# Kernel optimization log

Measured on AMD Instinct MI355X. Metric: run time of the kernel, lower is better.

Reference implementation:

```python
import jax, jax.numpy as jnp
import numpy as np

DIM = 3072
HEADS = 24
HD = 128
FF = 4 * DIM
EPS = 1e-6
SCALE_SHIFT = 1.0


def _ln(x):
    # LayerNorm, elementwise_affine=False
    mu = jnp.mean(x, axis=-1, keepdims=True)
    var = jnp.mean(jnp.square(x - mu), axis=-1, keepdims=True)
    return (x - mu) * jax.lax.rsqrt(var + EPS)


def _rms(x, w):
    # RMSNorm over head_dim with learned weight
    ms = jnp.mean(jnp.square(x), axis=-1, keepdims=True)
    return x * jax.lax.rsqrt(ms + EPS) * w


def _rope(x, cos, sin):
    # x: [B,S,H,D], cos/sin: [S,D]; interleaved rotate-half (diffusers style)
    xr = x.reshape(*x.shape[:-1], -1, 2)
    x1, x2 = xr[..., 0], xr[..., 1]
    rot = jnp.stack([-x2, x1], axis=-1).reshape(x.shape)
    return x * cos[None, :, None, :] + rot * sin[None, :, None, :]


def _mod_params(temb, w, b):
    m = jax.nn.silu(temb) @ w + b  # [B, 6*DIM]
    B = m.shape[0]
    m = m.reshape(B, -1, 6).transpose(0, 2, 1).reshape(B, -1)  # reorder to 6 blocks of DIM
    return jnp.split(m, 2, axis=-1)  # mod1, mod2 each [B, 3*DIM]


def _modulate(x, mp):
    shift, scale, gate = jnp.split(mp, 3, axis=-1)
    scale = scale + SCALE_SHIFT
    return x * scale[:, None, :] + shift[:, None, :], gate[:, None, :]


def setup_inputs() -> dict:
    key = jax.random.key(0)
    ks = jax.random.split(key, 32)
    B, ST, SI = 1, 512, 1024
    S = ST + SI
    r = lambda k, shp, s=1.0: jax.random.normal(k, shp, dtype=jnp.float32) * s
    W = 0.02  # weight init scale
    ang = jax.random.uniform(ks[5], (S, HD), minval=0.0, maxval=2 * np.pi)
    inp = {
        "hidden_states": r(ks[0], (B, SI, DIM)),
        "encoder_hidden_states": r(ks[1], (B, ST, DIM)),
        "encoder_hidden_states_mask": jnp.ones((B, ST), jnp.float32),
        "temb": r(ks[2], (B, DIM)),
        "rope_cos": jnp.cos(ang),
        "rope_sin": jnp.sin(ang),
        "w_img_mod": r(ks[6], (DIM, 6 * DIM), W), "b_img_mod": r(ks[7], (6 * DIM,), W),
        "w_txt_mod": r(ks[8], (DIM, 6 * DIM), W), "b_txt_mod": r(ks[9], (6 * DIM,), W),
        "norm_q_w": jnp.ones((HD,), jnp.float32), "norm_k_w": jnp.ones((HD,), jnp.float32),
        "norm_added_q_w": jnp.ones((HD,), jnp.float32), "norm_added_k_w": jnp.ones((HD,), jnp.float32),
        "w_qkv": r(ks[10], (DIM, 3 * DIM), W), "b_qkv": r(ks[11], (3 * DIM,), W),
        "w_add_qkv": r(ks[12], (DIM, 3 * DIM), W), "b_add_qkv": r(ks[13], (3 * DIM,), W),
        "w_out": r(ks[14], (DIM, DIM), W), "b_out": r(ks[15], (DIM,), W),
        "w_add_out": r(ks[16], (DIM, DIM), W), "b_add_out": r(ks[17], (DIM,), W),
        "w_img_mlp1": r(ks[18], (DIM, FF), W), "b_img_mlp1": r(ks[19], (FF,), W),
        "w_img_mlp2": r(ks[20], (FF, DIM), W), "b_img_mlp2": r(ks[21], (DIM,), W),
        "w_txt_mlp1": r(ks[22], (DIM, FF), W), "b_txt_mlp1": r(ks[23], (FF,), W),
        "w_txt_mlp2": r(ks[24], (FF, DIM), W), "b_txt_mlp2": r(ks[25], (DIM,), W),
    }
    return inp


def reference(hidden_states, encoder_hidden_states, encoder_hidden_states_mask, temb,
              rope_cos, rope_sin,
              w_img_mod, b_img_mod, w_txt_mod, b_txt_mod,
              norm_q_w, norm_k_w, norm_added_q_w, norm_added_k_w,
              w_qkv, b_qkv, w_add_qkv, b_add_qkv,
              w_out, b_out, w_add_out, b_add_out,
              w_img_mlp1, b_img_mlp1, w_img_mlp2, b_img_mlp2,
              w_txt_mlp1, b_txt_mlp1, w_txt_mlp2, b_txt_mlp2):
    B, SI, _ = hidden_states.shape
    ST = encoder_hidden_states.shape[1]

    img_mod1, img_mod2 = _mod_params(temb, w_img_mod, b_img_mod)
    txt_mod1, txt_mod2 = _mod_params(temb, w_txt_mod, b_txt_mod)

    img_m, img_g1 = _modulate(_ln(hidden_states), img_mod1)
    txt_m, txt_g1 = _modulate(_ln(encoder_hidden_states), txt_mod1)

    # joint attention
    iq, ik, iv = jnp.split(img_m @ w_qkv + b_qkv, 3, axis=-1)
    tq, tk, tv = jnp.split(txt_m @ w_add_qkv + b_add_qkv, 3, axis=-1)
    iq = _rms(iq.reshape(B, SI, HEADS, HD), norm_q_w)
    ik = _rms(ik.reshape(B, SI, HEADS, HD), norm_k_w)
    iv = iv.reshape(B, SI, HEADS, HD)
    tq = _rms(tq.reshape(B, ST, HEADS, HD), norm_added_q_w)
    tk = _rms(tk.reshape(B, ST, HEADS, HD), norm_added_k_w)
    tv = tv.reshape(B, ST, HEADS, HD)
    q = jnp.concatenate([tq, iq], axis=1)  # [B,S,H,D], txt first
    k = jnp.concatenate([tk, ik], axis=1)
    v = jnp.concatenate([tv, iv], axis=1)
    q = _rope(q, rope_cos, rope_sin)
    k = _rope(k, rope_cos, rope_sin)
    scores = jnp.einsum('bqhd,bkhd->bhqk', q, k) / np.float32(np.sqrt(HD))
    probs = jax.nn.softmax(scores, axis=-1)
    attn = jnp.einsum('bhqk,bkhd->bqhd', probs, v).reshape(B, ST + SI, HEADS * HD)

    txt_a = attn[:, :ST] @ w_add_out + b_add_out
    img_a = attn[:, ST:] @ w_out + b_out
    hidden = hidden_states + img_g1 * img_a
    enc = encoder_hidden_states + txt_g1 * txt_a

    # fused GELU(tanh) MLPs with modulation
    img_m2, img_g2 = _modulate(_ln(hidden), img_mod2)
    img_mlp = jax.nn.gelu(img_m2 @ w_img_mlp1 + b_img_mlp1, approximate=True) @ w_img_mlp2 + b_img_mlp2
    hidden = hidden + img_g2 * img_mlp

    txt_m2, txt_g2 = _modulate(_ln(enc), txt_mod2)
    txt_mlp = jax.nn.gelu(txt_m2 @ w_txt_mlp1 + b_txt_mlp1, approximate=True) @ w_txt_mlp2 + b_txt_mlp2
    enc = enc + txt_g2 * txt_mlp

    return enc, hidden
```

## Files before the change

kernel.cpp:

```cpp
#include <hip/hip_runtime.h>

#define DIMX 3072
#define STX 512
#define SIX 1024
#define SQX 1536
#define FFX 12288

typedef __attribute__((ext_vector_type(4))) float f32x4;
typedef __attribute__((ext_vector_type(8))) __bf16 bf16x8;
typedef __attribute__((ext_vector_type(4))) int i32x4;
typedef __attribute__((ext_vector_type(4))) unsigned short u16x4;

__device__ __forceinline__ unsigned short f2bf(float f){
  unsigned u = __builtin_bit_cast(unsigned, f);
  u += 0x7FFFu + ((u>>16)&1u);
  return (unsigned short)(u>>16);
}
__device__ __forceinline__ unsigned short usbf(float x){
  return __builtin_bit_cast(unsigned short, (__bf16)x);
}
__device__ __forceinline__ float bf2f(unsigned short h){
  unsigned u = ((unsigned)h)<<16;
  return __builtin_bit_cast(float, u);
}
__device__ __forceinline__ float gelu_tanh(float x){
  float x3 = x*x*x;
  float z = 0.7978845608028654f*(x + 0.044715f*x3);
  z = fminf(fmaxf(z, -15.f), 15.f);
  float e = exp2f(z*2.8853900817779268f);
  float th = (e-1.f)/(e+1.f);
  return 0.5f*x*(1.f+th);
}

__device__ __forceinline__ void gload16(const void* g, void* l){
  __builtin_amdgcn_global_load_lds(
      (const __attribute__((address_space(1))) void*)g,
      (__attribute__((address_space(3))) void*)l,
      16, 0, 0);
}


__global__ void k_silu(const float* __restrict__ temb, float* __restrict__ out){
  int i = blockIdx.x*256 + threadIdx.x;
  if(i < DIMX){
    float x = temb[i];
    out[i] = x / (1.f + exp2f(-x*1.4426950408889634f));
  }
}

__global__ void k_modinit(const float* __restrict__ b_img, const float* __restrict__ b_txt,
                          float* __restrict__ mod){
  int idx = blockIdx.x*256 + threadIdx.x;
  int mat = idx / 18432; int r = idx % 18432;
  int i = r/6, j = r%6;
  const float* b = mat ? b_txt : b_img;
  mod[mat*18432 + j*3072 + i] = b[r];
}

__global__ void k_modgemv(const float* __restrict__ w_img, const float* __restrict__ w_txt,
                          const float* __restrict__ silu_t, float* __restrict__ mod){
  int bz = blockIdx.x;
  int ks = bz & 7; bz >>= 3;
  int nc = bz % 18; int mat = bz / 18;
  const float* W = mat ? w_txt : w_img;
  __shared__ float st[384];
  int k0 = ks*384;
  for(int i = threadIdx.x; i < 384; i += 256) st[i] = silu_t[k0+i];
  __syncthreads();
  int n0 = nc*1024 + threadIdx.x*4;
  float ax=0.f, ay=0.f, az=0.f, aw=0.f;
  const float* Wp = W + (size_t)k0*18432 + n0;
  #pragma unroll 4
  for(int k=0;k<384;k++){
    float4 w = *(const float4*)(Wp + (size_t)k*18432);
    float s = st[k];
    ax += s*w.x; ay += s*w.y; az += s*w.z; aw += s*w.w;
  }
  float* md = mod + mat*18432;
  float vals[4] = {ax, ay, az, aw};
  #pragma unroll
  for(int j=0;j<4;j++){
    int n = n0+j; int i = n/6, jj = n%6;
    atomicAdd(&md[jj*3072 + i], vals[j]);
  }
}

__global__ void k_initC2(float* __restrict__ out0, const float* __restrict__ res0,
                         const float* __restrict__ gate0, const float* __restrict__ bias0,
                         float* __restrict__ out1, const float* __restrict__ res1,
                         const float* __restrict__ gate1, const float* __restrict__ bias1,
                         int R0){
  long i = ((long)blockIdx.x*256 + threadIdx.x)*4;
  int row = (int)(i / 3072);
  int col = (int)(i % 3072);
  const float* res; const float* gate; const float* bias; float* out;
  long off;
  if(row < R0){ res=res0; gate=gate0; bias=bias0; out=out0; off=i; }
  else        { res=res1; gate=gate1; bias=bias1; out=out1; off=i - (long)R0*3072; }
  float4 r = *(const float4*)(res + off);
  float4 g = *(const float4*)(gate + col);
  float4 b = *(const float4*)(bias + col);
  float4 o = {r.x + g.x*b.x, r.y + g.y*b.y, r.z + g.z*b.z, r.w + g.w*b.w};
  *(float4*)(out + off) = o;
}

__global__ void k_lnmod2(const float* __restrict__ x0, const float* __restrict__ modp0,
                         unsigned short* __restrict__ out0,
                         const float* __restrict__ x1, const float* __restrict__ modp1,
                         unsigned short* __restrict__ out1, int R0){
  int row = blockIdx.x, t = threadIdx.x;
  const float* x; const float* modp; unsigned short* out;
  if(row < R0){ x=x0; modp=modp0; out=out0; }
  else        { x=x1; modp=modp1; out=out1; row -= R0; }
  const float* xr = x + (size_t)row*DIMX;
  float4 v0 = *(const float4*)(xr + t*4);
  float4 v1 = *(const float4*)(xr + 1024 + t*4);
  float4 v2 = *(const float4*)(xr + 2048 + t*4);
  float s  = v0.x+v0.y+v0.z+v0.w + v1.x+v1.y+v1.z+v1.w + v2.x+v2.y+v2.z+v2.w;
  float s2 = v0.x*v0.x+v0.y*v0.y+v0.z*v0.z+v0.w*v0.w
           + v1.x*v1.x+v1.y*v1.y+v1.z*v1.z+v1.w*v1.w
           + v2.x*v2.x+v2.y*v2.y+v2.z*v2.z+v2.w*v2.w;
  #pragma unroll
  for(int o=32;o>0;o>>=1){ s += __shfl_xor(s,o); s2 += __shfl_xor(s2,o); }
  __shared__ float rs_[4], rs2_[4];
  int wid = t>>6;
  if((t&63)==0){ rs_[wid]=s; rs2_[wid]=s2; }
  __syncthreads();
  float S  = rs_[0]+rs_[1]+rs_[2]+rs_[3];
  float S2 = rs2_[0]+rs2_[1]+rs2_[2]+rs2_[3];
  float mu = S*(1.f/3072.f);
  float var = S2*(1.f/3072.f) - mu*mu;
  float rstd = rsqrtf(var + 1e-6f);
  #pragma unroll
  for(int j=0;j<3;j++){
    int c = j*1024 + t*4;
    float4 sh = *(const float4*)(modp + c);
    float4 sc = *(const float4*)(modp + 3072 + c);
    float4 xv = (j==0)?v0:((j==1)?v1:v2);
    unsigned short h0 = f2bf((xv.x-mu)*rstd*(sc.x+1.f)+sh.x);
    unsigned short h1 = f2bf((xv.y-mu)*rstd*(sc.y+1.f)+sh.y);
    unsigned short h2 = f2bf((xv.z-mu)*rstd*(sc.z+1.f)+sh.z);
    unsigned short h3 = f2bf((xv.w-mu)*rstd*(sc.w+1.f)+sh.w);
    unsigned long long pk = (unsigned long long)(h0 | ((unsigned)h1<<16))
                          | ((unsigned long long)(h2 | ((unsigned)h3<<16))<<32);
    *(unsigned long long*)(out + (size_t)row*DIMX + c) = pk;
  }
}

__global__ void k_rmsrope(const unsigned short* __restrict__ qkv_txt,
                          const unsigned short* __restrict__ qkv_img,
                          const float* __restrict__ nqw, const float* __restrict__ nkw,
                          const float* __restrict__ naqw, const float* __restrict__ nakw,
                          const float* __restrict__ cosb, const float* __restrict__ sinb,
                          unsigned short* __restrict__ Q, unsigned short* __restrict__ K,
                          unsigned short* __restrict__ V){
  int s = blockIdx.x, h = blockIdx.y, t = threadIdx.x;
  bool txt = s < STX;
  const unsigned short* src = txt ? (qkv_txt + (size_t)s*9216)
                                  : (qkv_img + (size_t)(s-STX)*9216);
  const float* qw = txt ? naqw : nqw;
  const float* kw = txt ? nakw : nkw;
  int d0 = 2*t;
  float q1 = bf2f(src[h*128 + d0]),        q2 = bf2f(src[h*128 + d0 + 1]);
  float k1 = bf2f(src[3072 + h*128 + d0]), k2 = bf2f(src[3072 + h*128 + d0 + 1]);
  float v1 = bf2f(src[6144 + h*128 + d0]), v2 = bf2f(src[6144 + h*128 + d0 + 1]);
  float sq = q1*q1 + q2*q2, sk = k1*k1 + k2*k2;
  #pragma unroll
  for(int o=32;o>0;o>>=1){ sq += __shfl_xor(sq,o); sk += __shfl_xor(sk,o); }
  float rq = rsqrtf(sq*(1.f/128.f) + 1e-6f);
  float rk = rsqrtf(sk*(1.f/128.f) + 1e-6f);
  q1 *= rq*qw[d0]; q2 *= rq*qw[d0+1];
  k1 *= rk*kw[d0]; k2 *= rk*kw[d0+1];
  float c1 = cosb[(size_t)s*128 + d0], c2 = cosb[(size_t)s*128 + d0 + 1];
  float s1 = sinb[(size_t)s*128 + d0], s2 = sinb[(size_t)s*128 + d0 + 1];
  float Q1 = q1*c1 - q2*s1, Q2 = q2*c2 + q1*s2;
  float K1 = k1*c1 - k2*s1, K2 = k2*c2 + k1*s2;
  size_t o = ((size_t)s*24 + h)*128 + d0;
  Q[o] = f2bf(Q1); Q[o+1] = f2bf(Q2);
  K[o] = f2bf(K1); K[o+1] = f2bf(K2);
  V[o] = f2bf(v1); V[o+1] = f2bf(v2);
}

__global__ void k_vtrans(const unsigned short* __restrict__ V, unsigned short* __restrict__ VT){
  __shared__ unsigned short tile[64][136];
  int st = blockIdx.x, h = blockIdx.y, t = threadIdx.x;
  int s0 = st*64;
  {
    int s = t>>2;
    #pragma unroll
    for(int i=0;i<4;i++){
      int oct = ((t&3)<<2) + i;
      i32x4 d = *(const i32x4*)(V + ((size_t)(s0+s)*24 + h)*128 + oct*8);
      *(i32x4*)&tile[s][oct*8] = d;
    }
  }
  __syncthreads();
  {
    int d0 = t>>3; int strip = t&7;
    #pragma unroll
    for(int i=0;i<4;i++){
      int d = d0 + i*32;
      unsigned short h8[8];
      #pragma unroll
      for(int j=0;j<8;j++) h8[j] = tile[strip*8 + j][d];
      unsigned a0 = h8[0] | ((unsigned)h8[1]<<16);
      unsigned a1 = h8[2] | ((unsigned)h8[3]<<16);
      unsigned a2 = h8[4] | ((unsigned)h8[5]<<16);
      unsigned a3 = h8[6] | ((unsigned)h8[7]<<16);
      i32x4 dv = {(int)a0,(int)a1,(int)a2,(int)a3};
      *(i32x4*)(VT + ((size_t)h*128 + d)*1536 + s0 + strip*8) = dv;
    }
  }
}

__global__ __launch_bounds__(256,2) void k_fattn(
    const unsigned short* __restrict__ Q,
    const unsigned short* __restrict__ Kb,
    const unsigned short* __restrict__ VT,
    unsigned short* __restrict__ O)
{
  __shared__ unsigned short Kls[4][64][32];
  __shared__ unsigned short Vls[2][128][32];
  __shared__ unsigned short Pls[128][72];
  const int t = threadIdx.x;
  const int qb = blockIdx.x, h = blockIdx.y;
  const int lane = t&63, w = t>>6;
  const int lr = lane&15, lk = lane>>4;
  const float SC  = 0.08838834764831845f;
  const float L2E = 1.4426950408889634f;
  const int schunk = ((lane&3) ^ ((lane>>2)&3))*8;
  const int rswz   = ((lr&3)<<3);

  bf16x8 qf[2][4];
  {
    const unsigned short* qp = Q + ((size_t)(qb*128 + w*32 + lr)*3072) + h*128 + lk*8;
    #pragma unroll
    for(int mf=0;mf<2;mf++)
      #pragma unroll
      for(int ks=0;ks<4;ks++)
        qf[mf][ks] = *(const bf16x8*)(qp + (size_t)mf*16*3072 + ks*32);
  }

  f32x4 o[2][8];
  #pragma unroll
  for(int i=0;i<2;i++)
    #pragma unroll
    for(int j=0;j<8;j++) o[i][j] = (f32x4){0.f,0.f,0.f,0.f};
  float mrow[2][4], lrow[2][4];
  #pragma unroll
  for(int i=0;i<2;i++)
    #pragma unroll
    for(int r=0;r<4;r++){ mrow[i][r] = -3.0e30f; lrow[i][r] = 0.f; }

  for(int kv0=0; kv0<SQX; kv0+=64){
    __syncthreads();
    {
      const unsigned short* kp = Kb + ((size_t)(kv0 + (lane>>2))*3072) + h*128 + w*32 + schunk;
      #pragma unroll
      for(int i=0;i<4;i++)
        gload16(kp + (size_t)i*16*3072, &Kls[w][i*16][0]);
    }
    {
      int c = w>>1;
      const unsigned short* vp = VT + ((size_t)(h*128 + (w&1)*64 + (lane>>2)))*1536 + kv0 + c*32 + schunk;
      #pragma unroll
      for(int j=0;j<4;j++)
        gload16(vp + (size_t)j*16*1536, &Vls[c][(w&1)*64 + j*16][0]);
    }
    __syncthreads();

    f32x4 s[2][4];
    #pragma unroll
    for(int mf=0;mf<2;mf++)
      #pragma unroll
      for(int nf=0;nf<4;nf++) s[mf][nf] = (f32x4){0.f,0.f,0.f,0.f};
    #pragma unroll
    for(int ks=0;ks<4;ks++){
      bf16x8 kf[4];
      #pragma unroll
      for(int nf=0;nf<4;nf++) kf[nf] = *(const bf16x8*)&Kls[ks][nf*16+lr][(lk*8) ^ rswz];
      #pragma unroll
      for(int mf=0;mf<2;mf++)
        #pragma unroll
        for(int nf=0;nf<4;nf++)
          s[mf][nf] = __builtin_amdgcn_mfma_f32_16x16x32_bf16(qf[mf][ks], kf[nf], s[mf][nf], 0,0,0);
    }

    #pragma unroll
    for(int mf=0;mf<2;mf++){
      #pragma unroll
      for(int r=0;r<4;r++){
        float v = fmaxf(fmaxf(s[mf][0][r], s[mf][1][r]), fmaxf(s[mf][2][r], s[mf][3][r]));
        #pragma unroll
        for(int d=1; d<16; d<<=1) v = fmaxf(v, __shfl_xor(v, d));
        float nm = fmaxf(mrow[mf][r], v*SC);
        float fac = exp2f((mrow[mf][r]-nm)*L2E);
        mrow[mf][r] = nm;
        float rs = 0.f;
        #pragma unroll
        for(int nf=0;nf<4;nf++){
          float p = exp2f((s[mf][nf][r]*SC - nm)*L2E);
          s[mf][nf][r] = p;
          rs += p;
        }
        #pragma unroll
        for(int d=1; d<16; d<<=1) rs += __shfl_xor(rs, d);
        lrow[mf][r] = lrow[mf][r]*fac + rs;
        #pragma unroll
        for(int nf=0;nf<8;nf++) o[mf][nf][r] *= fac;
      }
    }

    #pragma unroll
    for(int mf=0;mf<2;mf++)
      #pragma unroll
      for(int nf=0;nf<4;nf++)
        #pragma unroll
        for(int r=0;r<4;r++)
          Pls[w*32 + mf*16 + lk*4 + r][nf*16 + lr] = usbf(s[mf][nf][r]);

    #pragma unroll
    for(int ks2=0; ks2<2; ks2++){
      bf16x8 pa[2];
      #pragma unroll
      for(int mf=0;mf<2;mf++)
        pa[mf] = *(const bf16x8*)&Pls[w*32 + mf*16 + lr][ks2*32 + lk*8];
      #pragma unroll
      for(int nf=0;nf<8;nf++){
        bf16x8 vf = *(const bf16x8*)&Vls[ks2][nf*16+lr][(lk*8) ^ rswz];
        #pragma unroll
        for(int mf=0;mf<2;mf++)
          o[mf][nf] = __builtin_amdgcn_mfma_f32_16x16x32_bf16(pa[mf], vf, o[mf][nf], 0,0,0);
      }
    }
  }

  #pragma unroll
  for(int mf=0;mf<2;mf++){
    float inv[4];
    #pragma unroll
    for(int r=0;r<4;r++) inv[r] = 1.f/lrow[mf][r];
    #pragma unroll
    for(int nf=0;nf<8;nf++){
      #pragma unroll
      for(int r=0;r<4;r++){
        size_t row = (size_t)qb*128 + w*32 + mf*16 + lk*4 + r;
        size_t col = (size_t)h*128 + nf*16 + lr;
        O[row*3072 + col] = usbf(o[mf][nf][r]*inv[r]);
      }
    }
  }
}

__global__ __launch_bounds__(256,4) void k_gemmW(
    const unsigned short* __restrict__ A0, const unsigned short* __restrict__ A1, long lda,
    const float* __restrict__ W0, const float* __restrict__ W1, long ldw,
    const float* __restrict__ bias0, const float* __restrict__ bias1,
    void* __restrict__ C0, void* __restrict__ C1, long ldc,
    int nM0, int K, int KS, int mode,
    const float* __restrict__ gate0, const float* __restrict__ gate1)
{
  __shared__ unsigned short Als[2][128*32];
  __shared__ unsigned short Bls[2][128*40];
  const int t = threadIdx.x;
  const int bn = blockIdx.x;
  int bm = blockIdx.y;
  const bool sel1 = (bm >= nM0);
  const unsigned short* A = sel1 ? A1 : A0;
  const float* W  = sel1 ? W1 : W0;
  const float* bias = sel1 ? bias1 : bias0;
  const float* gate = sel1 ? gate1 : gate0;
  void* Cp = sel1 ? C1 : C0;
  if(sel1) bm -= nM0;
  const int zs = blockIdx.z;
  const int Kc = K / KS, kbeg = zs*Kc, kend = kbeg + Kc;

  const unsigned short* Ab = A + (size_t)bm*128*lda;
  const float* Wb = W + (size_t)bn*128;

  const int lane = t & 63, wid = t>>6, wr = wid>>1, wc = wid&1;
  const int lr = lane & 15, lk = lane>>4;
  const int srow = (lane>>2);
  const int soff = (((lane&3) ^ ((lane>>2)&3))*8);
  const int aswz = (lk*8) ^ ((lr&3)<<3);
  const int bswz = (lk*8) ^ (((lr>>2)&3)<<3);
  const int u = t&31, v = t>>5;
  const int wcol = (v*4) ^ ((u&3)<<3);

  f32x4 acc[4][4];
  #pragma unroll
  for(int i=0;i<4;i++)
    #pragma unroll
    for(int j=0;j<4;j++) acc[i][j] = {0.f,0.f,0.f,0.f};

  float4 wreg[4];

  gload16(Ab + (size_t)(     wid*16 + srow)*lda + kbeg + soff, &Als[0][(     wid*16)*32]);
  gload16(Ab + (size_t)(64 + wid*16 + srow)*lda + kbeg + soff, &Als[0][(64 + wid*16)*32]);
  #pragma unroll
  for(int j=0;j<4;j++)
    wreg[j] = *(const float4*)(Wb + (size_t)(kbeg + v*4 + j)*ldw + u*4);
  #pragma unroll
  for(int i=0;i<4;i++){
    u16x4 pk = { usbf(wreg[0][i]), usbf(wreg[1][i]), usbf(wreg[2][i]), usbf(wreg[3][i]) };
    *(u16x4*)&Bls[0][(u*4+i)*40 + wcol] = pk;
  }
  __syncthreads();

  unsigned short* AlsC = &Als[0][0]; unsigned short* AlsN = &Als[1][0];
  unsigned short* BlsC = &Bls[0][0]; unsigned short* BlsN = &Bls[1][0];

  for(int k0=kbeg; k0<kend; k0+=32){
    const bool has = (k0 + 32 < kend);
    if(has){
      int kn = k0 + 32;
      gload16(Ab + (size_t)(     wid*16 + srow)*lda + kn + soff, AlsN + (     wid*16)*32);
      gload16(Ab + (size_t)(64 + wid*16 + srow)*lda + kn + soff, AlsN + (64 + wid*16)*32);
      #pragma unroll
      for(int j=0;j<4;j++)
        wreg[j] = *(const float4*)(Wb + (size_t)(kn + v*4 + j)*ldw + u*4);
    }
    {
      bf16x8 af[4], bfr[4];
      #pragma unroll
      for(int mf=0;mf<4;mf++) af[mf]  = *(const bf16x8*)&AlsC[(wr*64 + mf*16 + lr)*32 + aswz];
      #pragma unroll
      for(int nf=0;nf<4;nf++) bfr[nf] = *(const bf16x8*)&BlsC[(wc*64 + nf*16 + lr)*40 + bswz];
      #pragma unroll
      for(int mf=0;mf<4;mf++)
        #pragma unroll
        for(int nf=0;nf<4;nf++)
          acc[mf][nf] = __builtin_amdgcn_mfma_f32_16x16x32_bf16(af[mf], bfr[nf], acc[mf][nf], 0,0,0);
    }
    if(has){
      #pragma unroll
      for(int i=0;i<4;i++){
        u16x4 pk = { usbf(wreg[0][i]), usbf(wreg[1][i]), usbf(wreg[2][i]), usbf(wreg[3][i]) };
        *(u16x4*)&BlsN[(u*4+i)*40 + wcol] = pk;
      }
    }
    __syncthreads();
    unsigned short* tmp;
    tmp = AlsC; AlsC = AlsN; AlsN = tmp;
    tmp = BlsC; BlsC = BlsN; BlsN = tmp;
  }

  unsigned short* C16 = (unsigned short*)Cp;
  float* C32 = (float*)Cp;
  #pragma unroll
  for(int mf=0;mf<4;mf++){
    #pragma unroll
    for(int nf=0;nf<4;nf++){
      #pragma unroll
      for(int r=0;r<4;r++){
        size_t row = (size_t)bm*128 + wr*64 + mf*16 + lk*4 + r;
        size_t col = (size_t)bn*128 + wc*64 + nf*16 + lr;
        float v2 = acc[mf][nf][r];
        if(mode==0){
          C16[row*ldc + col] = f2bf(v2 + (bias ? bias[col] : 0.f));
        } else if(mode==1){
          C16[row*ldc + col] = f2bf(gelu_tanh(v2 + (bias ? bias[col] : 0.f)));
        } else {
          float g = gate ? gate[col] : 1.f;
          atomicAdd(&C32[row*ldc + col], g*v2);
        }
      }
    }
  }
}


extern "C" void kernel_launch(void* const* d_in, const int* in_sizes, int n_in,
                              void* d_out, int out_size, void* d_ws, size_t ws_size,
                              hipStream_t stream){
  const float* hidden_states = (const float*)d_in[0];
  const float* enc_states    = (const float*)d_in[1];
  const float* temb          = (const float*)d_in[3];
  const float* rope_cos      = (const float*)d_in[4];
  const float* rope_sin      = (const float*)d_in[5];
  const float* w_img_mod     = (const float*)d_in[6];
  const float* b_img_mod     = (const float*)d_in[7];
  const float* w_txt_mod     = (const float*)d_in[8];
  const float* b_txt_mod     = (const float*)d_in[9];
  const float* norm_q_w      = (const float*)d_in[10];
  const float* norm_k_w      = (const float*)d_in[11];
  const float* norm_aq_w     = (const float*)d_in[12];
  const float* norm_ak_w     = (const float*)d_in[13];
  const float* w_qkv   = (const float*)d_in[14];
  const float* b_qkv   = (const float*)d_in[15];
  const float* w_aqkv  = (const float*)d_in[16];
  const float* b_aqkv  = (const float*)d_in[17];
  const float* w_out_  = (const float*)d_in[18];
  const float* b_out_  = (const float*)d_in[19];
  const float* w_aout  = (const float*)d_in[20];
  const float* b_aout  = (const float*)d_in[21];
  const float* w_mlp1i = (const float*)d_in[22];
  const float* b_mlp1i = (const float*)d_in[23];
  const float* w_mlp2i = (const float*)d_in[24];
  const float* b_mlp2i = (const float*)d_in[25];
  const float* w_mlp1t = (const float*)d_in[26];
  const float* b_mlp1t = (const float*)d_in[27];
  const float* w_mlp2t = (const float*)d_in[28];
  const float* b_mlp2t = (const float*)d_in[29];

  char* ws = (char*)d_ws;
  float* mod    = (float*)(ws + 0);
  float* silu_t = (float*)(ws + 147456);
  unsigned short* imgm = (unsigned short*)(ws + 159744);
  unsigned short* txtm = (unsigned short*)(ws + 6451200);
  float* hid = (float*)(ws + 9596928);
  float* enc = (float*)(ws + 22179840);
  unsigned short* Qb  = (unsigned short*)(ws + 47345664);
  unsigned short* Kb  = (unsigned short*)(ws + 56782848);
  unsigned short* Vb  = (unsigned short*)(ws + 66220032);
  unsigned short* attnb = (unsigned short*)(ws + 66220032);
  unsigned short* VTb = (unsigned short*)(ws + 75657216);
  unsigned short* mlphI = (unsigned short*)(ws + 103968768);
  unsigned short* mlphT = (unsigned short*)(ws + 129134592);
  unsigned short* qkvi = (unsigned short*)(ws + 141717504);
  unsigned short* qkvt = (unsigned short*)(ws + 160591872);

  float* out_enc = (float*)d_out;
  float* out_hid = (float*)d_out + (size_t)STX*DIMX;

  k_silu<<<12,256,0,stream>>>(temb, silu_t);
  k_modinit<<<144,256,0,stream>>>(b_img_mod, b_txt_mod, mod);
  k_modgemv<<<288,256,0,stream>>>(w_img_mod, w_txt_mod, silu_t, mod);

  k_lnmod2<<<SQX,256,0,stream>>>(hidden_states, mod + 0, imgm,
                                 enc_states, mod + 18432, txtm, SIX);

  k_gemmW<<<dim3(72,12,1),256,0,stream>>>(imgm, txtm, 3072,
      w_qkv, w_aqkv, 9216, b_qkv, b_aqkv,
      qkvi, qkvt, 9216, 8, 3072,1, 0, nullptr,nullptr);

  k_rmsrope<<<dim3(1536,24),64,0,stream>>>(qkvt, qkvi, norm_q_w, norm_k_w,
      norm_aq_w, norm_ak_w, rope_cos, rope_sin, Qb, Kb, Vb);
  k_vtrans<<<dim3(24,24),256,0,stream>>>(Vb, VTb);

  k_fattn<<<dim3(12,24),256,0,stream>>>(Qb, Kb, VTb, attnb);

  k_initC2<<<4608,256,0,stream>>>(hid, hidden_states, mod + 2*3072, b_out_,
                                  enc, enc_states, mod + 18432 + 2*3072, b_aout, SIX);
  k_gemmW<<<dim3(24,12,4),256,0,stream>>>(attnb + (size_t)512*3072, attnb, 3072,
      w_out_, w_aout, 3072, nullptr, nullptr,
      hid, enc, 3072, 8, 3072,4, 3, mod + 2*3072, mod + 18432 + 2*3072);

  k_lnmod2<<<SQX,256,0,stream>>>(hid, mod + 3*3072, imgm,
                                 enc, mod + 18432 + 3*3072, txtm, SIX);

  k_gemmW<<<dim3(96,12,1),256,0,stream>>>(imgm, txtm, 3072,
      w_mlp1i, w_mlp1t, 12288, b_mlp1i, b_mlp1t,
      mlphI, mlphT, 12288, 8, 3072,1, 1, nullptr,nullptr);

  k_initC2<<<4608,256,0,stream>>>(out_hid, hid, mod + 5*3072, b_mlp2i,
                                  out_enc, enc, mod + 18432 + 5*3072, b_mlp2t, SIX);
  k_gemmW<<<dim3(24,12,4),256,0,stream>>>(mlphI, mlphT, 12288,
      w_mlp2i, w_mlp2t, 3072, nullptr, nullptr,
      out_hid, out_enc, 3072, 8, 12288,4, 3, mod + 5*3072, mod + 18432 + 5*3072);
}
```

Measured before the change: 1.103 ms.

## Deepen GEMM weight prefetch to two stages with explicit waitcnt barriers

Restructures the bf16 GEMM main loop, which reads fp32 weights, into a manually unrolled two-step pipeline. Weight register loads are issued two K-tiles ahead, using alternating register sets and fixed LDS buffer indices. Explicit s_waitcnt vmcnt(4) waits and sched_barriers replace __syncthreads so that weight loads stay in flight across the barrier. It also changes the LDS swizzle for A and drops the swizzle on B. The added register pressure and the hand-tuned waitcnt counts could cost occupancy or introduce correctness hazards.

```diff
diff --git a/kernel.cpp b/kernel.cpp
--- a/kernel.cpp
+++ b/kernel.cpp
@@ -381,11 +381,10 @@
   const int lane = t & 63, wid = t>>6, wr = wid>>1, wc = wid&1;
   const int lr = lane & 15, lk = lane>>4;
   const int srow = (lane>>2);
-  const int soff = (((lane&3) ^ ((lane>>2)&3))*8);
-  const int aswz = (lk*8) ^ ((lr&3)<<3);
-  const int bswz = (lk*8) ^ (((lr>>2)&3)<<3);
-  const int u = t&31, v = t>>5;
-  const int wcol = (v*4) ^ ((u&3)<<3);
+  const int soff = (((lane&3) ^ ((lane>>3)&3))*8);
+  const int aswz = ((lk ^ ((lr>>1)&3))*8);
+  const int u_ = t & 31;
+  const int v_ = t >> 5;
 
   f32x4 acc[4][4];
   #pragma unroll
@@ -393,57 +392,77 @@
     #pragma unroll
     for(int j=0;j<4;j++) acc[i][j] = {0.f,0.f,0.f,0.f};
 
-  float4 wreg[4];
-
-  gload16(Ab + (size_t)(     wid*16 + srow)*lda + kbeg + soff, &Als[0][(     wid*16)*32]);
-  gload16(Ab + (size_t)(64 + wid*16 + srow)*lda + kbeg + soff, &Als[0][(64 + wid*16)*32]);
-  #pragma unroll
-  for(int j=0;j<4;j++)
-    wreg[j] = *(const float4*)(Wb + (size_t)(kbeg + v*4 + j)*ldw + u*4);
-  #pragma unroll
-  for(int i=0;i<4;i++){
-    u16x4 pk = { usbf(wreg[0][i]), usbf(wreg[1][i]), usbf(wreg[2][i]), usbf(wreg[3][i]) };
-    *(u16x4*)&Bls[0][(u*4+i)*40 + wcol] = pk;
-  }
-  __syncthreads();
-
-  unsigned short* AlsC = &Als[0][0]; unsigned short* AlsN = &Als[1][0];
-  unsigned short* BlsC = &Bls[0][0]; unsigned short* BlsN = &Bls[1][0];
-
-  for(int k0=kbeg; k0<kend; k0+=32){
-    const bool has = (k0 + 32 < kend);
-    if(has){
-      int kn = k0 + 32;
-      gload16(Ab + (size_t)(     wid*16 + srow)*lda + kn + soff, AlsN + (     wid*16)*32);
-      gload16(Ab + (size_t)(64 + wid*16 + srow)*lda + kn + soff, AlsN + (64 + wid*16)*32);
-      #pragma unroll
-      for(int j=0;j<4;j++)
-        wreg[j] = *(const float4*)(Wb + (size_t)(kn + v*4 + j)*ldw + u*4);
-    }
+  float4 wE[4], wO[4];
+
+#define GW_ISSUE_A(KT, DST) \
+  gload16(Ab + (size_t)(     wid*16 + srow)*lda + (KT) + soff, (DST) + (     wid*16)*32); \
+  gload16(Ab + (size_t)(64 + wid*16 + srow)*lda + (KT) + soff, (DST) + (64 + wid*16)*32);
+
+#define GW_LOAD_W(KT, WS) \
+  { _Pragma("unroll") \
+    for(int j=0;j<4;j++) WS[j] = *(const float4*)(Wb + (size_t)((KT) + v_*4 + j)*ldw + u_*4); }
+
+#define GW_PACK(WS, DST) \
+  { _Pragma("unroll") \
+    for(int i=0;i<4;i++){ \
+      u16x4 pk = { usbf(WS[0][i]), usbf(WS[1][i]), usbf(WS[2][i]), usbf(WS[3][i]) }; \
+      *(u16x4*)&(DST)[(u_*4+i)*40 + v_*4] = pk; \
+    } }
+
+#define GW_MFMA(ALS, BLS) \
+  { bf16x8 af[4], bfr[4]; \
+    _Pragma("unroll") \
+    for(int mf=0;mf<4;mf++) af[mf]  = *(const bf16x8*)&(ALS)[(wr*64 + mf*16 + lr)*32 + aswz]; \
+    _Pragma("unroll") \
+    for(int nf=0;nf<4;nf++) bfr[nf] = *(const bf16x8*)&(BLS)[(wc*64 + nf*16 + lr)*40 + lk*8]; \
+    _Pragma("unroll") \
+    for(int mf=0;mf<4;mf++) \
+      _Pragma("unroll") \
+      for(int nf=0;nf<4;nf++) \
+        acc[mf][nf] = __builtin_amdgcn_mfma_f32_16x16x32_bf16(af[mf], bfr[nf], acc[mf][nf], 0,0,0); }
+
+  GW_LOAD_W(kbeg, wE);
+  GW_PACK(wE, Bls[0]);
+  GW_ISSUE_A(kbeg, Als[0]);
+  __builtin_amdgcn_sched_barrier(0);
+  GW_LOAD_W(kbeg+32, wO);
+  asm volatile("s_waitcnt vmcnt(4) lgkmcnt(0)" ::: "memory");
+  __builtin_amdgcn_s_barrier();
+
+  for(int k0=kbeg; k0<kend; k0+=64){
     {
-      bf16x8 af[4], bfr[4];
-      #pragma unroll
-      for(int mf=0;mf<4;mf++) af[mf]  = *(const bf16x8*)&AlsC[(wr*64 + mf*16 + lr)*32 + aswz];
-      #pragma unroll
-      for(int nf=0;nf<4;nf++) bfr[nf] = *(const bf16x8*)&BlsC[(wc*64 + nf*16 + lr)*40 + bswz];
-      #pragma unroll
-      for(int mf=0;mf<4;mf++)
-        #pragma unroll
-        for(int nf=0;nf<4;nf++)
-          acc[mf][nf] = __builtin_amdgcn_mfma_f32_16x16x32_bf16(af[mf], bfr[nf], acc[mf][nf], 0,0,0);
-    }
-    if(has){
-      #pragma unroll
-      for(int i=0;i<4;i++){
-        u16x4 pk = { usbf(wreg[0][i]), usbf(wreg[1][i]), usbf(wreg[2][i]), usbf(wreg[3][i]) };
-        *(u16x4*)&BlsN[(u*4+i)*40 + wcol] = pk;
+      GW_ISSUE_A(k0+32, Als[1]);
+      __builtin_amdgcn_sched_barrier(0);
+      const bool hW = (k0+64 < kend);
+      if(hW){ GW_LOAD_W(k0+64, wE); }
+      GW_MFMA(Als[0], Bls[0]);
+      GW_PACK(wO, Bls[1]);
+      if(hW) asm volatile("s_waitcnt vmcnt(4) lgkmcnt(0)" ::: "memory");
+      else   asm volatile("s_waitcnt vmcnt(0) lgkmcnt(0)" ::: "memory");
+      __builtin_amdgcn_s_barrier();
+    }
+    {
+      const bool hA = (k0+64 < kend);
+      const bool hW2 = (k0+96 < kend);
+      if(hA){
+        GW_ISSUE_A(k0+64, Als[0]);
+        __builtin_amdgcn_sched_barrier(0);
       }
-    }
-    __syncthreads();
-    unsigned short* tmp;
-    tmp = AlsC; AlsC = AlsN; AlsN = tmp;
-    tmp = BlsC; BlsC = BlsN; BlsN = tmp;
-  }
+      if(hW2){ GW_LOAD_W(k0+96, wO); }
+      GW_MFMA(Als[1], Bls[1]);
+      if(hA){
+        GW_PACK(wE, Bls[0]);
+        if(hW2) asm volatile("s_waitcnt vmcnt(4) lgkmcnt(0)" ::: "memory");
+        else    asm volatile("s_waitcnt vmcnt(0) lgkmcnt(0)" ::: "memory");
+        __builtin_amdgcn_s_barrier();
+      }
+    }
+  }
+
+#undef GW_ISSUE_A
+#undef GW_LOAD_W
+#undef GW_PACK
+#undef GW_MFMA
 
   unsigned short* C16 = (unsigned short*)Cp;
   float* C32 = (float*)Cp;
```

After: 1.765 ms. 60.0% more time.
